# Performance work log

Hardware: AMD Instinct MI355X
Metric: run time of the kernel (lower is better)

The kernel has to match this reference:

```python
import jax, jax.numpy as jnp
import numpy as np

N_NODES = 100000
N_EDGES = 1200000
NODE_DIM = 128
HIDDEN = 64
N_POSTS = 50000


def setup_inputs() -> dict:
    key = jax.random.key(0)
    ks = jax.random.split(key, 10)
    s = 1.0 / np.sqrt(NODE_DIM)
    sh = 1.0 / np.sqrt(HIDDEN)
    return {
        "node_features": jax.random.normal(ks[0], (N_NODES, NODE_DIM), dtype=jnp.float32),
        "edge_index": jax.random.randint(ks[1], (2, N_EDGES), 0, N_NODES, dtype=jnp.int64) if jax.config.jax_enable_x64 else jax.random.randint(ks[1], (2, N_EDGES), 0, N_NODES, dtype=jnp.int32),
        "post_mask": jax.random.randint(ks[2], (N_POSTS,), 0, N_NODES, dtype=jnp.int32),
        "W_enc": jax.random.uniform(ks[3], (NODE_DIM, HIDDEN), jnp.float32, -s, s),
        "b_enc": jax.random.uniform(ks[4], (HIDDEN,), jnp.float32, -s, s),
        "W_conv": jax.random.uniform(ks[5], (HIDDEN, HIDDEN), jnp.float32, -sh, sh),
        "b_conv": jax.random.uniform(ks[6], (HIDDEN,), jnp.float32, -sh, sh),
        "W_out": jax.random.uniform(ks[7], (HIDDEN, 1), jnp.float32, -sh, sh),
        "b_out": jax.random.uniform(ks[8], (1,), jnp.float32, -sh, sh),
    }


def reference(node_features, edge_index, post_mask, W_enc, b_enc, W_conv, b_conv, W_out, b_out):
    # encode: relu(Linear)
    node_emb = jax.nn.relu(node_features @ W_enc + b_enc)  # [N, H]
    src, dst = edge_index[0], edge_index[1]
    # per-edge gather then scatter-add into destination nodes (segment sum)
    messages = jax.ops.segment_sum(node_emb[src], dst, num_segments=node_emb.shape[0])  # [N, H]
    node_emb = jax.nn.relu((node_emb + messages) @ W_conv + b_conv)  # [N, H]
    post_emb = node_emb[post_mask]  # [P, H]
    out = jax.nn.sigmoid((post_emb @ W_out + b_out).squeeze(-1))  # [P]
    return out
```

## Files before the change

### kernel.cpp

```cpp
#include <hip/hip_runtime.h>
#include <hip/hip_bf16.h>
#include <math.h>


#define HIDDEN 64
#define NODE_DIM 128
#define SCAN_CHUNK 1024

typedef __attribute__((ext_vector_type(8))) short short8;
typedef __attribute__((ext_vector_type(4))) float floatx4;

union F2B { short8 s; __hip_bfloat162 h[4]; };
union B2U { __hip_bfloat16 b; unsigned short u; };

__device__ inline short8 cvt8(const float4& p, const float4& q) {
    F2B u;
    u.h[0] = __float22bfloat162_rn(make_float2(p.x, p.y));
    u.h[1] = __float22bfloat162_rn(make_float2(p.z, p.w));
    u.h[2] = __float22bfloat162_rn(make_float2(q.x, q.y));
    u.h[3] = __float22bfloat162_rn(make_float2(q.z, q.w));
    return u.s;
}

__device__ inline void cvt8_split(const float4& p, const float4& q,
                                  short8& hi, short8& lo) {
    const float f[8] = {p.x, p.y, p.z, p.w, q.x, q.y, q.z, q.w};
    F2B uh, ul;
    #pragma unroll
    for (int jj = 0; jj < 4; ++jj) {
        const float2 v = make_float2(f[2 * jj], f[2 * jj + 1]);
        const __hip_bfloat162 h = __float22bfloat162_rn(v);
        const float2 hv = __bfloat1622float2(h);
        ul.h[jj] = __float22bfloat162_rn(make_float2(v.x - hv.x, v.y - hv.y));
        uh.h[jj] = h;
    }
    hi = uh.s; lo = ul.s;
}

__global__ __launch_bounds__(256) void k_pre(
    const int* __restrict__ post, unsigned int* __restrict__ bits,
    int* __restrict__ nodelist, int* __restrict__ listCnt,
    int* __restrict__ count, int n_posts, int n_nodes)
{
    const int gtid = blockIdx.x * 256 + threadIdx.x;
    if (gtid < n_nodes) count[gtid] = 0;
    if (gtid < n_posts) {
        const int n = post[gtid];
        const unsigned int bit = 1u << (n & 31);
        const unsigned int old = atomicOr(&bits[n >> 5], bit);
        if (!(old & bit)) {
            const int i = atomicAdd(listCnt, 1);
            nodelist[i] = n;
        }
    }
}

__global__ __launch_bounds__(256) void k_encode_count(
    const float* __restrict__ A, const float* __restrict__ We,
    const float* __restrict__ be, __hip_bfloat16* __restrict__ emb16,
    const int* __restrict__ dsts, const unsigned int* __restrict__ bits,
    int* __restrict__ count, int* __restrict__ rank,
    int n_nodes, int n_tiles, int n_edges)
{
    __shared__ unsigned short sW16[NODE_DIM * HIDDEN];

    {
        const float4* src = (const float4*)We;
        #pragma unroll
        for (int i = 0; i < 8; ++i) {
            const int fidx = i * 256 + threadIdx.x;
            const float4 v = src[fidx];
            #pragma unroll
            for (int c = 0; c < 4; ++c) {
                const int linear = fidx * 4 + c;
                const int k   = linear >> 6;
                const int col = linear & 63;
                const int ks   = k >> 5;
                const int kw   = k & 31;
                const int quad = kw >> 3;
                const int jj   = (kw & 7) >> 1;
                const int b    = kw & 1;
                const int nt   = col >> 4;
                const int r    = col & 15;
                const int dst = ((((ks * 4 + nt) * 4 + quad) * 16 + r) * 8) + jj * 2 + b;
                const float fv = (c == 0) ? v.x : (c == 1) ? v.y : (c == 2) ? v.z : v.w;
                B2U cv; cv.b = __float2bfloat16(fv);
                sW16[dst] = cv.u;
            }
        }
    }
    __syncthreads();

    const int lane = threadIdx.x & 63;
    const int r    = lane & 15;
    const int quad = lane >> 4;

    short8 Wb[4][4];
    #pragma unroll
    for (int ks = 0; ks < 4; ++ks)
        #pragma unroll
        for (int nt = 0; nt < 4; ++nt)
            Wb[ks][nt] = *(const short8*)&sW16[(((ks * 4 + nt) * 4 + quad) * 16 + r) * 8];

    float bias[4];
    #pragma unroll
    for (int nt = 0; nt < 4; ++nt) bias[nt] = be[nt * 16 + r];

    const int wid    = (blockIdx.x * 256 + threadIdx.x) >> 6;
    const int nwaves = gridDim.x * 4;

    const int estride = gridDim.x * 256;
    int e = blockIdx.x * 256 + threadIdx.x;

    for (int t = wid; t < n_tiles; t += nwaves) {
        const float* Arow = A + (size_t)t * 16 * NODE_DIM + (size_t)r * NODE_DIM + quad * 8;
        float4 a[4][2];
        #pragma unroll
        for (int ks = 0; ks < 4; ++ks) {
            a[ks][0] = *(const float4*)(Arow + ks * 32);
            a[ks][1] = *(const float4*)(Arow + ks * 32 + 4);
        }

        #pragma unroll
        for (int q = 0; q < 3; ++q) {
            if (e < n_edges) {
                const int d = dsts[e];
                if ((bits[d >> 5] >> (d & 31)) & 1u)
                    rank[e] = atomicAdd(&count[d], 1);
                e += estride;
            }
        }

        floatx4 acc[4] = {};
        #pragma unroll
        for (int ks = 0; ks < 4; ++ks) {
            const short8 af = cvt8(a[ks][0], a[ks][1]);
            #pragma unroll
            for (int nt = 0; nt < 4; ++nt)
                acc[nt] = __builtin_amdgcn_mfma_f32_16x16x32_bf16(af, Wb[ks][nt], acc[nt], 0, 0, 0);
        }
        #pragma unroll
        for (int nt = 0; nt < 4; ++nt)
            #pragma unroll
            for (int g = 0; g < 4; ++g) {
                const int node = t * 16 + quad * 4 + g;
                const float h = fmaxf(acc[nt][g] + bias[nt], 0.0f);
                emb16[(size_t)node * HIDDEN + nt * 16 + r] = __float2bfloat16(h);
            }
    }
    const int rem = n_nodes - n_tiles * 16;
    if (rem > 0 && wid == 0) {
        for (int n = n_tiles * 16; n < n_nodes; ++n) {
            float acc = be[lane];
            const float* row = A + (size_t)n * NODE_DIM;
            for (int k = 0; k < NODE_DIM; ++k)
                acc = fmaf(row[k], We[(size_t)k * HIDDEN + lane], acc);
            emb16[(size_t)n * HIDDEN + lane] = __float2bfloat16(fmaxf(acc, 0.0f));
        }
    }

    for (; e < n_edges; e += estride) {
        const int d = dsts[e];
        if ((bits[d >> 5] >> (d & 31)) & 1u)
            rank[e] = atomicAdd(&count[d], 1);
    }
}

__global__ __launch_bounds__(256) void k_scan_lb(
    const int* __restrict__ count, int* __restrict__ row_start,
    unsigned int* __restrict__ partials, int n)
{
    __shared__ int s[256];
    __shared__ int sExc;
    const int b = blockIdx.x, tid = threadIdx.x;
    const int base = b * SCAN_CHUNK + tid * 4;
    int c0 = (base + 0 < n) ? count[base + 0] : 0;
    int c1 = (base + 1 < n) ? count[base + 1] : 0;
    int c2 = (base + 2 < n) ? count[base + 2] : 0;
    int c3 = (base + 3 < n) ? count[base + 3] : 0;
    const int t = c0 + c1 + c2 + c3;
    s[tid] = t;
    __syncthreads();
    #pragma unroll
    for (int off = 1; off < 256; off <<= 1) {
        int v = (tid >= off) ? s[tid - off] : 0;
        __syncthreads();
        s[tid] += v;
        __syncthreads();
    }
    const int total = s[255];

    if (b == 0) {
        if (tid == 0) {
            __hip_atomic_store(&partials[0], (2u << 30) | (unsigned int)total,
                               __ATOMIC_RELEASE, __HIP_MEMORY_SCOPE_AGENT);
            sExc = 0;
        }
    } else {
        if (tid == 0) {
            __hip_atomic_store(&partials[b], (1u << 30) | (unsigned int)total,
                               __ATOMIC_RELEASE, __HIP_MEMORY_SCOPE_AGENT);
        }
        if (tid < 64) {
            int exc = 0;
            int winEnd = b;
            while (true) {
                const int j = winEnd - 64 + tid;
                const unsigned int v = (j >= 0)
                    ? __hip_atomic_load(&partials[j], __ATOMIC_ACQUIRE,
                                        __HIP_MEMORY_SCOPE_AGENT)
                    : (2u << 30);
                const unsigned int st = v >> 30;
                if (__ballot(st == 0u)) {
                    __builtin_amdgcn_s_sleep(1);
                    continue;
                }
                const unsigned long long b2 = __ballot(st == 2u);
                int contrib;
                bool done;
                if (b2) {
                    const int hi = 63 - __clzll(b2);
                    contrib = (tid >= hi) ? (int)(v & 0x3FFFFFFFu) : 0;
                    done = true;
                } else {
                    contrib = (int)(v & 0x3FFFFFFFu);
                    done = false;
                }
                #pragma unroll
                for (int off = 1; off < 64; off <<= 1)
                    contrib += __shfl_xor(contrib, off);
                exc += contrib;
                if (done) break;
                winEnd -= 64;
            }
            if (tid == 0) {
                __hip_atomic_store(&partials[b],
                                   (2u << 30) | (unsigned int)(exc + total),
                                   __ATOMIC_RELEASE, __HIP_MEMORY_SCOPE_AGENT);
                sExc = exc;
            }
        }
    }
    __syncthreads();
    int run = sExc + s[tid] - t;
    if (base + 0 < n) row_start[base + 0] = run;           run += c0;
    if (base + 1 < n) row_start[base + 1] = run;           run += c1;
    if (base + 2 < n) row_start[base + 2] = run;           run += c2;
    if (base + 3 < n) row_start[base + 3] = run;
}

__global__ __launch_bounds__(256) void k_fill(
    const int* __restrict__ srcs, const int* __restrict__ dsts,
    const unsigned int* __restrict__ bits, const int* __restrict__ row_start,
    const int* __restrict__ rank, int* __restrict__ slots, int n_edges)
{
    const int stride = gridDim.x * 256;
    for (int e = blockIdx.x * 256 + threadIdx.x; e < n_edges; e += stride) {
        const int d = dsts[e];
        if (!((bits[d >> 5] >> (d & 31)) & 1u)) continue;
        slots[row_start[d] + rank[e]] = srcs[e];
    }
}

__global__ __launch_bounds__(256) void k_gather_head(
    const int* __restrict__ nodelist, const int* __restrict__ listCnt,
    const int* __restrict__ row_start, const int* __restrict__ count,
    const int* __restrict__ slots, const __hip_bfloat16* __restrict__ emb16,
    const float* __restrict__ Wc, const float* __restrict__ bc,
    const float* __restrict__ Wo, const float* __restrict__ bo,
    float* __restrict__ res)
{
    const int lane = threadIdx.x & 63;
    const int r    = lane & 15;
    const int quad = lane >> 4;

    short8 Wb[2][4];
    #pragma unroll
    for (int ks = 0; ks < 2; ++ks)
        #pragma unroll
        for (int nt = 0; nt < 4; ++nt) {
            F2B u;
            #pragma unroll
            for (int jj = 0; jj < 4; ++jj) {
                const int k0 = ks * 32 + quad * 8 + 2 * jj;
                const float lo = Wc[(size_t)k0 * HIDDEN + nt * 16 + r];
                const float hi = Wc[(size_t)(k0 + 1) * HIDDEN + nt * 16 + r];
                u.h[jj] = __float22bfloat162_rn(make_float2(lo, hi));
            }
            Wb[ks][nt] = u.s;
        }
    float bias[4], wo[4];
    #pragma unroll
    for (int nt = 0; nt < 4; ++nt) { bias[nt] = bc[nt * 16 + r]; wo[nt] = Wo[nt * 16 + r]; }
    const float bo_s = bo[0];

    const int nc      = listCnt[0];
    const int n_tiles = (nc + 15) / 16;
    const int wid     = (blockIdx.x * 256 + threadIdx.x) >> 6;
    const int nwaves  = gridDim.x * 4;

    for (int tile = wid; tile < n_tiles; tile += nwaves) {
        const int i0  = tile * 16;
        const int row = i0 + r;

        float4 f0a = make_float4(0.f, 0.f, 0.f, 0.f), f0b = f0a;
        float4 f1a = f0a, f1b = f0a;
        if (row < nc) {
            const int n    = nodelist[row];
            const int m    = count[n];
            const int base = row_start[n];
            const size_t o0 = (size_t)n * HIDDEN + quad * 8;

            #define ACC2(vlo, vhi) do {                                          \
                F2B ua, ub; ua.s = (vlo); ub.s = (vhi); float2 t2;               \
                t2 = __bfloat1622float2(ua.h[0]); f0a.x += t2.x; f0a.y += t2.y;  \
                t2 = __bfloat1622float2(ua.h[1]); f0a.z += t2.x; f0a.w += t2.y;  \
                t2 = __bfloat1622float2(ua.h[2]); f0b.x += t2.x; f0b.y += t2.y;  \
                t2 = __bfloat1622float2(ua.h[3]); f0b.z += t2.x; f0b.w += t2.y;  \
                t2 = __bfloat1622float2(ub.h[0]); f1a.x += t2.x; f1a.y += t2.y;  \
                t2 = __bfloat1622float2(ub.h[1]); f1a.z += t2.x; f1a.w += t2.y;  \
                t2 = __bfloat1622float2(ub.h[2]); f1b.x += t2.x; f1b.y += t2.y;  \
                t2 = __bfloat1622float2(ub.h[3]); f1b.z += t2.x; f1b.w += t2.y;  \
            } while (0)

            {
                const short8 vlo = *(const short8*)(emb16 + o0);
                const short8 vhi = *(const short8*)(emb16 + o0 + 32);
                ACC2(vlo, vhi);
            }
            int c = 0;
            for (; c + 3 < m; c += 4) {
                const int s0 = slots[base + c];
                const int s1 = slots[base + c + 1];
                const int s2 = slots[base + c + 2];
                const int s3 = slots[base + c + 3];
                const size_t a0 = (size_t)s0 * HIDDEN + quad * 8;
                const size_t a1 = (size_t)s1 * HIDDEN + quad * 8;
                const size_t a2 = (size_t)s2 * HIDDEN + quad * 8;
                const size_t a3 = (size_t)s3 * HIDDEN + quad * 8;
                const short8 v0lo = *(const short8*)(emb16 + a0);
                const short8 v0hi = *(const short8*)(emb16 + a0 + 32);
                const short8 v1lo = *(const short8*)(emb16 + a1);
                const short8 v1hi = *(const short8*)(emb16 + a1 + 32);
                const short8 v2lo = *(const short8*)(emb16 + a2);
                const short8 v2hi = *(const short8*)(emb16 + a2 + 32);
                const short8 v3lo = *(const short8*)(emb16 + a3);
                const short8 v3hi = *(const short8*)(emb16 + a3 + 32);
                ACC2(v0lo, v0hi);
                ACC2(v1lo, v1hi);
                ACC2(v2lo, v2hi);
                ACC2(v3lo, v3hi);
            }
            for (; c < m; ++c) {
                const int s0 = slots[base + c];
                const size_t a0 = (size_t)s0 * HIDDEN + quad * 8;
                const short8 v0lo = *(const short8*)(emb16 + a0);
                const short8 v0hi = *(const short8*)(emb16 + a0 + 32);
                ACC2(v0lo, v0hi);
            }
            #undef ACC2
        }

        floatx4 acc[4] = {};
        {
            short8 ah, al;
            cvt8_split(f0a, f0b, ah, al);
            #pragma unroll
            for (int nt = 0; nt < 4; ++nt) {
                acc[nt] = __builtin_amdgcn_mfma_f32_16x16x32_bf16(ah, Wb[0][nt], acc[nt], 0, 0, 0);
                acc[nt] = __builtin_amdgcn_mfma_f32_16x16x32_bf16(al, Wb[0][nt], acc[nt], 0, 0, 0);
            }
            cvt8_split(f1a, f1b, ah, al);
            #pragma unroll
            for (int nt = 0; nt < 4; ++nt) {
                acc[nt] = __builtin_amdgcn_mfma_f32_16x16x32_bf16(ah, Wb[1][nt], acc[nt], 0, 0, 0);
                acc[nt] = __builtin_amdgcn_mfma_f32_16x16x32_bf16(al, Wb[1][nt], acc[nt], 0, 0, 0);
            }
        }
        float r4[4];
        #pragma unroll
        for (int gg = 0; gg < 4; ++gg) {
            float part = 0.0f;
            #pragma unroll
            for (int nt = 0; nt < 4; ++nt)
                part += fmaxf(acc[nt][gg] + bias[nt], 0.0f) * wo[nt];
            part += __shfl_xor(part, 1);
            part += __shfl_xor(part, 2);
            part += __shfl_xor(part, 4);
            part += __shfl_xor(part, 8);
            r4[gg] = part;
        }
        if (r == 0) {
            #pragma unroll
            for (int gg = 0; gg < 4; ++gg) {
                const int idx = i0 + quad * 4 + gg;
                if (idx < nc)
                    res[nodelist[idx]] = 1.0f / (1.0f + __expf(-(r4[gg] + bo_s)));
            }
        }
    }
}

__global__ __launch_bounds__(256) void k_out(
    const int* __restrict__ post, const float* __restrict__ res,
    float* __restrict__ out, int n_posts)
{
    const int p = blockIdx.x * 256 + threadIdx.x;
    if (p < n_posts) out[p] = res[post[p]];
}

extern "C" void kernel_launch(void* const* d_in, const int* in_sizes, int n_in,
                              void* d_out, int out_size, void* d_ws, size_t ws_size,
                              hipStream_t stream) {
    const float* A    = (const float*)d_in[0];
    const int*   ei   = (const int*)  d_in[1];
    const int*   post = (const int*)  d_in[2];
    const float* We   = (const float*)d_in[3];
    const float* be   = (const float*)d_in[4];
    const float* Wc   = (const float*)d_in[5];
    const float* bc   = (const float*)d_in[6];
    const float* Wo   = (const float*)d_in[7];
    const float* bo   = (const float*)d_in[8];
    float* out = (float*)d_out;

    const int n_nodes = in_sizes[0] / NODE_DIM;
    const int n_edges = in_sizes[1] / 2;
    const int n_posts = in_sizes[2];

    char* p = (char*)d_ws;
    __hip_bfloat16* emb16 = (__hip_bfloat16*)p;  p += (size_t)n_nodes * HIDDEN * 2;
    int*   slots    = (int*)p;                p += (size_t)n_edges * 4;
    int*   rank     = (int*)p;                p += (size_t)n_edges * 4;
    char* zbase = p;
    unsigned int* bits = (unsigned int*)p;    p += ((size_t)(n_nodes + 31) / 32 + 32) * 4;
    int*   listCnt  = (int*)p;                p += 256;
    unsigned int* partials = (unsigned int*)p; p += 1024;
    const size_t zbytes = (size_t)(p - zbase);
    int*   count    = (int*)p;                p += (size_t)n_nodes * 4;
    int*   row_start= (int*)p;                p += (size_t)n_nodes * 4;
    int*   nodelist = (int*)p;                p += (size_t)n_nodes * 4;
    float* res      = (float*)p;              p += (size_t)n_nodes * 4;

    const int* srcs = ei;
    const int* dsts = ei + n_edges;
    const int nb = (n_nodes + SCAN_CHUNK - 1) / SCAN_CHUNK;
    const int n_tiles = n_nodes / 16;

    (void)hipMemsetAsync(zbase, 0, zbytes, stream);
    k_pre<<<(n_nodes + 255) / 256, 256, 0, stream>>>(post, bits, nodelist, listCnt, count, n_posts, n_nodes);
    k_encode_count<<<1536, 256, 0, stream>>>(A, We, be, emb16, dsts, bits, count, rank, n_nodes, n_tiles, n_edges);
    k_scan_lb<<<nb, 256, 0, stream>>>(count, row_start, partials, n_nodes);
    k_fill<<<2048, 256, 0, stream>>>(srcs, dsts, bits, row_start, rank, slots, n_edges);
    k_gather_head<<<2048, 256, 0, stream>>>(nodelist, listCnt, row_start, count, slots, emb16, Wc, bc, Wo, bo, res);
    k_out<<<(n_posts + 255) / 256, 256, 0, stream>>>(post, res, out, n_posts);
}
```

Baseline: 183.1 us.

## Privatize per-node edge counters into four copies to reduce atomic contention

```diff
diff --git a/kernel.cpp b/kernel.cpp
--- a/kernel.cpp
+++ b/kernel.cpp
@@ -6,6 +6,7 @@
 #define HIDDEN 64
 #define NODE_DIM 128
 #define SCAN_CHUNK 1024
+#define NCOPY 4
 
 typedef __attribute__((ext_vector_type(8))) short short8;
 typedef __attribute__((ext_vector_type(4))) float floatx4;
@@ -43,7 +44,11 @@
     int* __restrict__ count, int n_posts, int n_nodes)
 {
     const int gtid = blockIdx.x * 256 + threadIdx.x;
-    if (gtid < n_nodes) count[gtid] = 0;
+    if (gtid < n_nodes) {
+        #pragma unroll
+        for (int c = 0; c < NCOPY; ++c)
+            count[c * n_nodes + gtid] = 0;
+    }
     if (gtid < n_posts) {
         const int n = post[gtid];
         const unsigned int bit = 1u << (n & 31);
@@ -111,6 +116,8 @@
 
     const int estride = gridDim.x * 256;
     int e = blockIdx.x * 256 + threadIdx.x;
+    int* mycount = count + (blockIdx.x & (NCOPY - 1)) * n_nodes;
+    const int ctag = (blockIdx.x & (NCOPY - 1)) << 28;
 
     for (int t = wid; t < n_tiles; t += nwaves) {
         const float* Arow = A + (size_t)t * 16 * NODE_DIM + (size_t)r * NODE_DIM + quad * 8;
@@ -126,7 +133,7 @@
             if (e < n_edges) {
                 const int d = dsts[e];
                 if ((bits[d >> 5] >> (d & 31)) & 1u)
-                    rank[e] = atomicAdd(&count[d], 1);
+                    rank[e] = ctag | atomicAdd(&mycount[d], 1);
                 e += estride;
             }
         }
@@ -162,22 +169,36 @@
     for (; e < n_edges; e += estride) {
         const int d = dsts[e];
         if ((bits[d >> 5] >> (d & 31)) & 1u)
-            rank[e] = atomicAdd(&count[d], 1);
+            rank[e] = ctag | atomicAdd(&mycount[d], 1);
     }
 }
 
 __global__ __launch_bounds__(256) void k_scan_lb(
-    const int* __restrict__ count, int* __restrict__ row_start,
-    unsigned int* __restrict__ partials, int n)
+    int* __restrict__ count, int* __restrict__ coff,
+    int* __restrict__ row_start, unsigned int* __restrict__ partials, int n)
 {
     __shared__ int s[256];
     __shared__ int sExc;
     const int b = blockIdx.x, tid = threadIdx.x;
     const int base = b * SCAN_CHUNK + tid * 4;
-    int c0 = (base + 0 < n) ? count[base + 0] : 0;
-    int c1 = (base + 1 < n) ? count[base + 1] : 0;
-    int c2 = (base + 2 < n) ? count[base + 2] : 0;
-    int c3 = (base + 3 < n) ? count[base + 3] : 0;
+
+    int tot[4] = {0, 0, 0, 0};
+    #pragma unroll
+    for (int q = 0; q < 4; ++q) {
+        const int node = base + q;
+        if (node < n) {
+            int c0 = count[0 * n + node];
+            int c1 = count[1 * n + node];
+            int c2 = count[2 * n + node];
+            int c3 = count[3 * n + node];
+            int4 off = make_int4(0, c0, c0 + c1, c0 + c1 + c2);
+            *(int4*)&coff[(size_t)node * 4] = off;
+            const int t = c0 + c1 + c2 + c3;
+            count[node] = t;
+            tot[q] = t;
+        }
+    }
+    const int c0 = tot[0], c1 = tot[1], c2 = tot[2], c3 = tot[3];
     const int t = c0 + c1 + c2 + c3;
     s[tid] = t;
     __syncthreads();
@@ -252,13 +273,17 @@
 __global__ __launch_bounds__(256) void k_fill(
     const int* __restrict__ srcs, const int* __restrict__ dsts,
     const unsigned int* __restrict__ bits, const int* __restrict__ row_start,
-    const int* __restrict__ rank, int* __restrict__ slots, int n_edges)
+    const int* __restrict__ rank, const int* __restrict__ coff,
+    int* __restrict__ slots, int n_edges)
 {
     const int stride = gridDim.x * 256;
     for (int e = blockIdx.x * 256 + threadIdx.x; e < n_edges; e += stride) {
         const int d = dsts[e];
         if (!((bits[d >> 5] >> (d & 31)) & 1u)) continue;
-        slots[row_start[d] + rank[e]] = srcs[e];
+        const unsigned int rv = (unsigned int)rank[e];
+        const int c = (int)(rv >> 28);
+        const int r = (int)(rv & 0x0FFFFFFFu);
+        slots[row_start[d] + coff[(size_t)d * 4 + c] + r] = srcs[e];
     }
 }
 
@@ -436,7 +461,8 @@
     int*   listCnt  = (int*)p;                p += 256;
     unsigned int* partials = (unsigned int*)p; p += 1024;
     const size_t zbytes = (size_t)(p - zbase);
-    int*   count    = (int*)p;                p += (size_t)n_nodes * 4;
+    int*   count    = (int*)p;                p += (size_t)NCOPY * n_nodes * 4;
+    int*   coff     = (int*)p;                p += (size_t)NCOPY * n_nodes * 4;
     int*   row_start= (int*)p;                p += (size_t)n_nodes * 4;
     int*   nodelist = (int*)p;                p += (size_t)n_nodes * 4;
     float* res      = (float*)p;              p += (size_t)n_nodes * 4;
@@ -449,8 +475,8 @@
     (void)hipMemsetAsync(zbase, 0, zbytes, stream);
     k_pre<<<(n_nodes + 255) / 256, 256, 0, stream>>>(post, bits, nodelist, listCnt, count, n_posts, n_nodes);
     k_encode_count<<<1536, 256, 0, stream>>>(A, We, be, emb16, dsts, bits, count, rank, n_nodes, n_tiles, n_edges);
-    k_scan_lb<<<nb, 256, 0, stream>>>(count, row_start, partials, n_nodes);
-    k_fill<<<2048, 256, 0, stream>>>(srcs, dsts, bits, row_start, rank, slots, n_edges);
+    k_scan_lb<<<nb, 256, 0, stream>>>(count, coff, row_start, partials, n_nodes);
+    k_fill<<<2048, 256, 0, stream>>>(srcs, dsts, bits, row_start, rank, coff, slots, n_edges);
     k_gather_head<<<2048, 256, 0, stream>>>(nodelist, listCnt, row_start, count, slots, emb16, Wc, bc, Wo, bo, res);
     k_out<<<(n_posts + 255) / 256, 256, 0, stream>>>(post, res, out, n_posts);
 }
```

Result: slower. 187.6 us (+2.4%).
